# Optimization experiments

Measured on AMD Instinct MI355X. Metric: run time of the kernel, lower is better.

## Reference

```python
import jax, jax.numpy as jnp
import numpy as np

N = 100000
E = 1600000
F_IN, F_HID, F_OUT = 128, 32, 2


def setup_inputs() -> dict:
    key = jax.random.key(0)
    k1, k2, k3, k4 = jax.random.split(key, 4)
    x = jax.random.normal(k1, (N, F_IN), dtype=jnp.float32)
    edge_index = jax.random.randint(k2, (2, E), 0, N, dtype=jnp.int64)
    # Glorot-style init like torch_geometric GCNConv
    W1 = jax.random.normal(k3, (F_IN, F_HID), dtype=jnp.float32) * (1.0 / np.sqrt(F_IN))
    b1 = jnp.zeros((F_HID,), dtype=jnp.float32)
    W2 = jax.random.normal(k4, (F_HID, F_OUT), dtype=jnp.float32) * (1.0 / np.sqrt(F_HID))
    b2 = jnp.zeros((F_OUT,), dtype=jnp.float32)
    return {"x": x, "edge_index": edge_index, "W1": W1, "b1": b1, "W2": W2, "b2": b2}


def _gcn_conv(x, row, col, norm, W, b):
    # GCNConv: transform, then normalized aggregate (source -> target), then bias
    h = x @ W                                   # [N, F_out]
    msg = norm[:, None] * h[row]                # gather + scale, [E+N, F_out]
    out = jax.ops.segment_sum(msg, col, num_segments=N)  # scatter-add to targets
    return out + b


def reference(x, edge_index, W1, b1, W2, b2):
    # add self-loops (GCNConv default)
    loops = jnp.arange(N, dtype=edge_index.dtype)
    row = jnp.concatenate([edge_index[0], loops])
    col = jnp.concatenate([edge_index[1], loops])
    # symmetric normalization: deg^{-1/2}[row] * deg^{-1/2}[col], deg = in-degree w/ self-loops
    deg = jax.ops.segment_sum(jnp.ones_like(col, dtype=x.dtype), col, num_segments=N)
    dinv = jnp.where(deg > 0, jax.lax.rsqrt(deg), 0.0)
    norm = dinv[row] * dinv[col]                # [E+N]

    h = _gcn_conv(x, row, col, norm, W1, b1)
    h = jax.nn.relu(h)
    h = _gcn_conv(h, row, col, norm, W2, b2)
    return jax.nn.log_softmax(h, axis=1)
```

## Files before the change

### kernel.cpp

```cpp
#include <hip/hip_runtime.h>
#include <hip/hip_bf16.h>
#include <math.h>
#include <stdint.h>


#define GNN_N 100000
#define GNN_E 1600000
#define NBUCK 391
#define CAP 4608
#define CH 4096

__global__ __launch_bounds__(256) void k_bucket(const int* __restrict__ row,
                                                const int* __restrict__ col,
                                                int* __restrict__ bucket_fill,
                                                uint32_t* __restrict__ slab, int e) {
    __shared__ int hist[NBUCK];
    __shared__ int base[NBUCK];
    const int tid = threadIdx.x;
    const int e0 = blockIdx.x * CH;
    const int m = min(CH, e - e0);
    const bool full = (m == CH);

    int cc[16], rr[16];
    for (int i = tid; i < NBUCK; i += 256) hist[i] = 0;
    __syncthreads();

    if (full) {
        #pragma unroll
        for (int t = 0; t < 16; ++t) {
            cc[t] = col[e0 + tid + t * 256];
            rr[t] = row[e0 + tid + t * 256];
        }
        #pragma unroll
        for (int t = 0; t < 16; ++t) atomicAdd(&hist[cc[t] >> 8], 1);
    } else {
        for (int i = tid; i < m; i += 256) atomicAdd(&hist[col[e0 + i] >> 8], 1);
    }
    __syncthreads();
    for (int i = tid; i < NBUCK; i += 256) {
        int bb = (i + blockIdx.x * 131) % NBUCK;
        base[bb] = atomicAdd(&bucket_fill[bb], hist[bb]);
    }
    __syncthreads();
    if (full) {
        #pragma unroll
        for (int t = 0; t < 16; ++t) {
            int b = cc[t] >> 8;
            int p = atomicAdd(&base[b], 1);
            if (p < CAP)
                slab[(size_t)b * CAP + p] = ((uint32_t)rr[t] << 8) | (uint32_t)(cc[t] & 255);
        }
    } else {
        for (int i = tid; i < m; i += 256) {
            int c = col[e0 + i];
            int r = row[e0 + i];
            int b = c >> 8;
            int p = atomicAdd(&base[b], 1);
            if (p < CAP)
                slab[(size_t)b * CAP + p] = ((uint32_t)r << 8) | (uint32_t)(c & 255);
        }
    }
}

__global__ __launch_bounds__(512) void k_bucket_scan(const int* __restrict__ bucket_fill,
                                                     int* __restrict__ bucket_base, int nb) {
    int tid = threadIdx.x;
    int v = (tid < nb) ? bucket_fill[tid] : 0;
    int lane = tid & 63, wave = tid >> 6;
    int inc = v;
    #pragma unroll
    for (int d = 1; d < 64; d <<= 1) {
        int t = __shfl_up(inc, d);
        if (lane >= d) inc += t;
    }
    __shared__ int wsum[8];
    if (lane == 63) wsum[wave] = inc;
    __syncthreads();
    if (tid == 0) {
        int a = 0;
        #pragma unroll
        for (int w = 0; w < 8; ++w) { int t = wsum[w]; wsum[w] = a; a += t; }
    }
    __syncthreads();
    if (tid < nb) bucket_base[tid] = inc - v + wsum[wave];
}

__global__ __launch_bounds__(512) void k_fine(const uint32_t* __restrict__ slab,
                                              const int* __restrict__ bucket_fill,
                                              const int* __restrict__ bucket_base,
                                              int* __restrict__ sorted_row,
                                              int* __restrict__ cnt,
                                              int* __restrict__ offsets,
                                              float* __restrict__ dinv, int n) {
    __shared__ int hist[256];
    __shared__ int excl[256];
    __shared__ int cur[256];
    __shared__ int wsum[4];
    __shared__ uint32_t stage[CAP];
    const int tid = threadIdx.x;
    const int b = blockIdx.x;
    const int nb = min(bucket_fill[b], CAP);
    const int gbase = bucket_base[b];
    const uint32_t* sl = slab + (size_t)b * CAP;

    if (tid < 256) { hist[tid] = 0; cur[tid] = 0; }
    __syncthreads();
    for (int i = tid; i < nb; i += 512)
        atomicAdd(&hist[sl[i] & 255u], 1);
    __syncthreads();
    int v = 0, inc = 0;
    const int lane = tid & 63, wave = tid >> 6;
    if (tid < 256) {
        v = hist[tid];
        inc = v;
        #pragma unroll
        for (int d = 1; d < 64; d <<= 1) {
            int t = __shfl_up(inc, d);
            if (lane >= d) inc += t;
        }
        if (lane == 63) wsum[wave] = inc;
    }
    __syncthreads();
    if (tid == 0) {
        int a = 0;
        #pragma unroll
        for (int w = 0; w < 4; ++w) { int t = wsum[w]; wsum[w] = a; a += t; }
    }
    __syncthreads();
    if (tid < 256) {
        int ex = inc - v + wsum[wave];
        excl[tid] = ex;
        int c = b * 256 + tid;
        if (c < n) {
            cnt[c] = v;
            offsets[c] = gbase + ex;
            dinv[c] = rsqrtf((float)(v + 1));
        }
    }
    __syncthreads();
    for (int i = tid; i < nb; i += 512) {
        uint32_t u = sl[i];
        int f = (int)(u & 255u);
        int p = atomicAdd(&cur[f], 1);
        stage[excl[f] + p] = u >> 8;
    }
    __syncthreads();
    for (int i = tid; i < nb; i += 512)
        sorted_row[gbase + i] = (int)stage[i];
}

__device__ inline uint32_t pack_bf16(float a, float b) {
    uint32_t ua = __float_as_uint(a);
    uint32_t ub = __float_as_uint(b);
    ua = (ua + 0x7fffu + ((ua >> 16) & 1u)) >> 16;
    ub = (ub + 0x7fffu + ((ub >> 16) & 1u)) >> 16;
    return ua | (ub << 16);
}
__device__ inline void bf8_acc(float* acc, uint4 u) {
    acc[0] += __uint_as_float(u.x << 16);
    acc[1] += __uint_as_float(u.x & 0xffff0000u);
    acc[2] += __uint_as_float(u.y << 16);
    acc[3] += __uint_as_float(u.y & 0xffff0000u);
    acc[4] += __uint_as_float(u.z << 16);
    acc[5] += __uint_as_float(u.z & 0xffff0000u);
    acc[6] += __uint_as_float(u.w << 16);
    acc[7] += __uint_as_float(u.w & 0xffff0000u);
}

#define MM1_NODES 64
__global__ __launch_bounds__(256) void k_matmul1(const float* __restrict__ x,
                                                 const float* __restrict__ W1,
                                                 const float* __restrict__ dinv,
                                                 uint32_t* __restrict__ h1s, int n) {
    __shared__ float xs[MM1_NODES * 129];
    __shared__ float w1s[128 * 32];
    const int tid = threadIdx.x;
    const int nodeBase = blockIdx.x * MM1_NODES;

    {
        const float4* w4 = (const float4*)W1;
        float4* s4 = (float4*)w1s;
        for (int i = tid; i < 1024; i += 256) s4[i] = w4[i];
    }
    {
        const float4* x4 = (const float4*)x;
        for (int i = tid; i < MM1_NODES * 32; i += 256) {
            int node = i >> 5;
            int k4 = i & 31;
            float4 v = make_float4(0.f, 0.f, 0.f, 0.f);
            if (nodeBase + node < n)
                v = x4[(size_t)(nodeBase + node) * 32 + k4];
            int bb = node * 129 + k4 * 4;
            xs[bb + 0] = v.x; xs[bb + 1] = v.y; xs[bb + 2] = v.z; xs[bb + 3] = v.w;
        }
    }
    __syncthreads();

    const int fg = tid & 7;
    const int ng = tid >> 3;
    const int n0 = ng * 2;
    float4 acc0 = make_float4(0.f, 0.f, 0.f, 0.f);
    float4 acc1 = make_float4(0.f, 0.f, 0.f, 0.f);
    const float4* w1s4 = (const float4*)w1s;
    const float* xr0 = &xs[n0 * 129];
    const float* xr1 = &xs[(n0 + 1) * 129];
    #pragma unroll 8
    for (int k = 0; k < 128; ++k) {
        float4 w = w1s4[k * 8 + fg];
        float a = xr0[k];
        float b = xr1[k];
        acc0.x += a * w.x; acc0.y += a * w.y; acc0.z += a * w.z; acc0.w += a * w.w;
        acc1.x += b * w.x; acc1.y += b * w.y; acc1.z += b * w.z; acc1.w += b * w.w;
    }
    int gn0 = nodeBase + n0;
    if (gn0 < n) {
        float d = dinv[gn0];
        uint2 o = make_uint2(pack_bf16(acc0.x * d, acc0.y * d),
                             pack_bf16(acc0.z * d, acc0.w * d));
        ((uint2*)h1s)[(size_t)gn0 * 8 + fg] = o;
    }
    if (gn0 + 1 < n) {
        float d = dinv[gn0 + 1];
        uint2 o = make_uint2(pack_bf16(acc1.x * d, acc1.y * d),
                             pack_bf16(acc1.z * d, acc1.w * d));
        ((uint2*)h1s)[(size_t)(gn0 + 1) * 8 + fg] = o;
    }
}

__global__ __launch_bounds__(256) void k_gather1(const int* __restrict__ offsets,
                                                 const int* __restrict__ cnt,
                                                 const int* __restrict__ sorted_row,
                                                 const uint32_t* __restrict__ h1s,
                                                 const float* __restrict__ dinv,
                                                 const float* __restrict__ b1,
                                                 const float* __restrict__ W2,
                                                 float* __restrict__ h2s, int n) {
    const int tid = threadIdx.x;
    const int l = tid & 3;
    const int node = blockIdx.x * 64 + (tid >> 2);
    if (node >= n) return;
    const uint4* h4 = (const uint4*)h1s;
    float acc[8], acc2[8];
    #pragma unroll
    for (int j = 0; j < 8; ++j) { acc[j] = 0.f; acc2[j] = 0.f; }
    bf8_acc(acc, h4[(size_t)node * 4 + l]);
    const int start = offsets[node];
    const int deg = cnt[node];
    int k = 0;
    for (; k + 2 <= deg; k += 2) {
        int r0 = sorted_row[start + k];
        int r1 = sorted_row[start + k + 1];
        uint4 ua = h4[(size_t)r0 * 4 + l];
        uint4 ub = h4[(size_t)r1 * 4 + l];
        bf8_acc(acc, ua);
        bf8_acc(acc2, ub);
    }
    if (k < deg) {
        int r = sorted_row[start + k];
        bf8_acc(acc, h4[(size_t)r * 4 + l]);
    }
    #pragma unroll
    for (int j = 0; j < 8; ++j) acc[j] += acc2[j];

    const float d = dinv[node];
    const int f0 = l * 8;
    float s0 = 0.f, s1 = 0.f;
    #pragma unroll
    for (int j = 0; j < 8; ++j) {
        float a = fmaxf(d * acc[j] + b1[f0 + j], 0.f);
        s0 += a * W2[(f0 + j) * 2];
        s1 += a * W2[(f0 + j) * 2 + 1];
    }
    s0 += __shfl_xor(s0, 1); s0 += __shfl_xor(s0, 2);
    s1 += __shfl_xor(s1, 1); s1 += __shfl_xor(s1, 2);
    if (l == 0) ((float2*)h2s)[node] = make_float2(d * s0, d * s1);
}

__global__ __launch_bounds__(256) void k_gather2(const int* __restrict__ offsets,
                                                 const int* __restrict__ cnt,
                                                 const int* __restrict__ sorted_row,
                                                 const float* __restrict__ h2s,
                                                 const float* __restrict__ dinv,
                                                 const float* __restrict__ b2,
                                                 float* __restrict__ out, int n) {
    const int tid = threadIdx.x;
    const int l = tid & 3;
    const int node = blockIdx.x * 64 + (tid >> 2);
    if (node >= n) return;
    const float2* h2 = (const float2*)h2s;
    float sx = 0.f, sy = 0.f;
    if (l == 0) { float2 s = h2[node]; sx = s.x; sy = s.y; }
    const int start = offsets[node];
    const int deg = cnt[node];
    for (int k = l; k < deg; k += 4) {
        float2 v = h2[sorted_row[start + k]];
        sx += v.x; sy += v.y;
    }
    sx += __shfl_xor(sx, 1); sx += __shfl_xor(sx, 2);
    sy += __shfl_xor(sy, 1); sy += __shfl_xor(sy, 2);
    if (l == 0) {
        float d = dinv[node];
        float v0 = d * sx + b2[0];
        float v1 = d * sy + b2[1];
        float m = fmaxf(v0, v1);
        float lg = m + logf(expf(v0 - m) + expf(v1 - m));
        ((float2*)out)[node] = make_float2(v0 - lg, v1 - lg);
    }
}

extern "C" void kernel_launch(void* const* d_in, const int* in_sizes, int n_in,
                              void* d_out, int out_size, void* d_ws, size_t ws_size,
                              hipStream_t stream) {
    const float* x  = (const float*)d_in[0];
    const int*   ei = (const int*)d_in[1];
    const float* W1 = (const float*)d_in[2];
    const float* b1 = (const float*)d_in[3];
    const float* W2 = (const float*)d_in[4];
    const float* b2 = (const float*)d_in[5];
    float* out = (float*)d_out;
    char* ws = (char*)d_ws;

    const int N = GNN_N, E = GNN_E;
    const int* row = ei;
    const int* col = ei + E;

    float*    dinv        = (float*)    ws;
    int*      cnt         = (int*)     (ws + 4ull *  100000);
    int*      offsets     = (int*)     (ws + 4ull *  200000);
    int*      bucket_fill = (int*)     (ws + 4ull *  300000);
    int*      bucket_base = (int*)     (ws + 4ull *  300512);
    int*      sorted_row  = (int*)     (ws + 4ull *  301024);
    float*    h2s         = (float*)   (ws + 4ull * 1901024);
    uint32_t* h1s         = (uint32_t*)(ws + 4ull * 2101024);
    uint32_t* slab        = (uint32_t*)(ws + 4ull * 3701024);

    hipMemsetAsync(bucket_fill, 0, NBUCK * sizeof(int), stream);

    k_bucket     <<<(E + CH - 1) / CH, 256, 0, stream>>>(row, col, bucket_fill, slab, E);
    k_bucket_scan<<<1, 512, 0, stream>>>(bucket_fill, bucket_base, NBUCK);
    k_fine       <<<NBUCK, 512, 0, stream>>>(slab, bucket_fill, bucket_base,
                                             sorted_row, cnt, offsets, dinv, N);
    k_matmul1    <<<(N + MM1_NODES - 1) / MM1_NODES, 256, 0, stream>>>(x, W1, dinv, h1s, N);
    k_gather1    <<<(N + 63) / 64, 256, 0, stream>>>(offsets, cnt, sorted_row, h1s, dinv, b1, W2, h2s, N);
    k_gather2    <<<(N + 63) / 64, 256, 0, stream>>>(offsets, cnt, sorted_row, h2s, dinv, b2, out, N);
}
```

Before: 188.0 us.

## Reorder pipeline: unscaled matmul first, fuse memset and bucket scan away

New measurement: 193.9 us. 1.03x slower.

```diff
diff --git a/kernel.cpp b/kernel.cpp
--- a/kernel.cpp
+++ b/kernel.cpp
@@ -8,146 +8,10 @@
 #define GNN_E 1600000
 #define NBUCK 391
 #define CAP 4608
-#define CH 4096
-
-__global__ __launch_bounds__(256) void k_bucket(const int* __restrict__ row,
-                                                const int* __restrict__ col,
-                                                int* __restrict__ bucket_fill,
-                                                uint32_t* __restrict__ slab, int e) {
-    __shared__ int hist[NBUCK];
-    __shared__ int base[NBUCK];
-    const int tid = threadIdx.x;
-    const int e0 = blockIdx.x * CH;
-    const int m = min(CH, e - e0);
-    const bool full = (m == CH);
-
-    int cc[16], rr[16];
-    for (int i = tid; i < NBUCK; i += 256) hist[i] = 0;
-    __syncthreads();
-
-    if (full) {
-        #pragma unroll
-        for (int t = 0; t < 16; ++t) {
-            cc[t] = col[e0 + tid + t * 256];
-            rr[t] = row[e0 + tid + t * 256];
-        }
-        #pragma unroll
-        for (int t = 0; t < 16; ++t) atomicAdd(&hist[cc[t] >> 8], 1);
-    } else {
-        for (int i = tid; i < m; i += 256) atomicAdd(&hist[col[e0 + i] >> 8], 1);
-    }
-    __syncthreads();
-    for (int i = tid; i < NBUCK; i += 256) {
-        int bb = (i + blockIdx.x * 131) % NBUCK;
-        base[bb] = atomicAdd(&bucket_fill[bb], hist[bb]);
-    }
-    __syncthreads();
-    if (full) {
-        #pragma unroll
-        for (int t = 0; t < 16; ++t) {
-            int b = cc[t] >> 8;
-            int p = atomicAdd(&base[b], 1);
-            if (p < CAP)
-                slab[(size_t)b * CAP + p] = ((uint32_t)rr[t] << 8) | (uint32_t)(cc[t] & 255);
-        }
-    } else {
-        for (int i = tid; i < m; i += 256) {
-            int c = col[e0 + i];
-            int r = row[e0 + i];
-            int b = c >> 8;
-            int p = atomicAdd(&base[b], 1);
-            if (p < CAP)
-                slab[(size_t)b * CAP + p] = ((uint32_t)r << 8) | (uint32_t)(c & 255);
-        }
-    }
-}
-
-__global__ __launch_bounds__(512) void k_bucket_scan(const int* __restrict__ bucket_fill,
-                                                     int* __restrict__ bucket_base, int nb) {
-    int tid = threadIdx.x;
-    int v = (tid < nb) ? bucket_fill[tid] : 0;
-    int lane = tid & 63, wave = tid >> 6;
-    int inc = v;
-    #pragma unroll
-    for (int d = 1; d < 64; d <<= 1) {
-        int t = __shfl_up(inc, d);
-        if (lane >= d) inc += t;
-    }
-    __shared__ int wsum[8];
-    if (lane == 63) wsum[wave] = inc;
-    __syncthreads();
-    if (tid == 0) {
-        int a = 0;
-        #pragma unroll
-        for (int w = 0; w < 8; ++w) { int t = wsum[w]; wsum[w] = a; a += t; }
-    }
-    __syncthreads();
-    if (tid < nb) bucket_base[tid] = inc - v + wsum[wave];
-}
-
-__global__ __launch_bounds__(512) void k_fine(const uint32_t* __restrict__ slab,
-                                              const int* __restrict__ bucket_fill,
-                                              const int* __restrict__ bucket_base,
-                                              int* __restrict__ sorted_row,
-                                              int* __restrict__ cnt,
-                                              int* __restrict__ offsets,
-                                              float* __restrict__ dinv, int n) {
-    __shared__ int hist[256];
-    __shared__ int excl[256];
-    __shared__ int cur[256];
-    __shared__ int wsum[4];
-    __shared__ uint32_t stage[CAP];
-    const int tid = threadIdx.x;
-    const int b = blockIdx.x;
-    const int nb = min(bucket_fill[b], CAP);
-    const int gbase = bucket_base[b];
-    const uint32_t* sl = slab + (size_t)b * CAP;
-
-    if (tid < 256) { hist[tid] = 0; cur[tid] = 0; }
-    __syncthreads();
-    for (int i = tid; i < nb; i += 512)
-        atomicAdd(&hist[sl[i] & 255u], 1);
-    __syncthreads();
-    int v = 0, inc = 0;
-    const int lane = tid & 63, wave = tid >> 6;
-    if (tid < 256) {
-        v = hist[tid];
-        inc = v;
-        #pragma unroll
-        for (int d = 1; d < 64; d <<= 1) {
-            int t = __shfl_up(inc, d);
-            if (lane >= d) inc += t;
-        }
-        if (lane == 63) wsum[wave] = inc;
-    }
-    __syncthreads();
-    if (tid == 0) {
-        int a = 0;
-        #pragma unroll
-        for (int w = 0; w < 4; ++w) { int t = wsum[w]; wsum[w] = a; a += t; }
-    }
-    __syncthreads();
-    if (tid < 256) {
-        int ex = inc - v + wsum[wave];
-        excl[tid] = ex;
-        int c = b * 256 + tid;
-        if (c < n) {
-            cnt[c] = v;
-            offsets[c] = gbase + ex;
-            dinv[c] = rsqrtf((float)(v + 1));
-        }
-    }
-    __syncthreads();
-    for (int i = tid; i < nb; i += 512) {
-        uint32_t u = sl[i];
-        int f = (int)(u & 255u);
-        int p = atomicAdd(&cur[f], 1);
-        stage[excl[f] + p] = u >> 8;
-    }
-    __syncthreads();
-    for (int i = tid; i < nb; i += 512)
-        sorted_row[gbase + i] = (int)stage[i];
-}
+#define CH 3125
+
+__device__ inline float bf_lo(uint32_t u) { return __uint_as_float(u << 16); }
+__device__ inline float bf_hi(uint32_t u) { return __uint_as_float(u & 0xffff0000u); }
 
 __device__ inline uint32_t pack_bf16(float a, float b) {
     uint32_t ua = __float_as_uint(a);
@@ -156,26 +20,26 @@
     ub = (ub + 0x7fffu + ((ub >> 16) & 1u)) >> 16;
     return ua | (ub << 16);
 }
-__device__ inline void bf8_acc(float* acc, uint4 u) {
-    acc[0] += __uint_as_float(u.x << 16);
-    acc[1] += __uint_as_float(u.x & 0xffff0000u);
-    acc[2] += __uint_as_float(u.y << 16);
-    acc[3] += __uint_as_float(u.y & 0xffff0000u);
-    acc[4] += __uint_as_float(u.z << 16);
-    acc[5] += __uint_as_float(u.z & 0xffff0000u);
-    acc[6] += __uint_as_float(u.w << 16);
-    acc[7] += __uint_as_float(u.w & 0xffff0000u);
+
+__device__ inline void bf8_fma(float* acc, uint4 u, float d) {
+    acc[0] += d * bf_lo(u.x); acc[1] += d * bf_hi(u.x);
+    acc[2] += d * bf_lo(u.y); acc[3] += d * bf_hi(u.y);
+    acc[4] += d * bf_lo(u.z); acc[5] += d * bf_hi(u.z);
+    acc[6] += d * bf_lo(u.w); acc[7] += d * bf_hi(u.w);
 }
 
 #define MM1_NODES 64
-__global__ __launch_bounds__(256) void k_matmul1(const float* __restrict__ x,
-                                                 const float* __restrict__ W1,
-                                                 const float* __restrict__ dinv,
-                                                 uint32_t* __restrict__ h1s, int n) {
+__global__ __launch_bounds__(256) void k_matmul1z(const float* __restrict__ x,
+                                                  const float* __restrict__ W1,
+                                                  uint32_t* __restrict__ h1u,
+                                                  int* __restrict__ bucket_fill, int n) {
     __shared__ float xs[MM1_NODES * 129];
     __shared__ float w1s[128 * 32];
     const int tid = threadIdx.x;
     const int nodeBase = blockIdx.x * MM1_NODES;
+
+    if (blockIdx.x == 0)
+        for (int i = tid; i < NBUCK; i += 256) bucket_fill[i] = 0;
 
     {
         const float4* w4 = (const float4*)W1;
@@ -213,24 +77,118 @@
         acc1.x += b * w.x; acc1.y += b * w.y; acc1.z += b * w.z; acc1.w += b * w.w;
     }
     int gn0 = nodeBase + n0;
-    if (gn0 < n) {
-        float d = dinv[gn0];
-        uint2 o = make_uint2(pack_bf16(acc0.x * d, acc0.y * d),
-                             pack_bf16(acc0.z * d, acc0.w * d));
-        ((uint2*)h1s)[(size_t)gn0 * 8 + fg] = o;
-    }
-    if (gn0 + 1 < n) {
-        float d = dinv[gn0 + 1];
-        uint2 o = make_uint2(pack_bf16(acc1.x * d, acc1.y * d),
-                             pack_bf16(acc1.z * d, acc1.w * d));
-        ((uint2*)h1s)[(size_t)(gn0 + 1) * 8 + fg] = o;
-    }
+    if (gn0 < n)
+        ((uint2*)h1u)[(size_t)gn0 * 8 + fg] =
+            make_uint2(pack_bf16(acc0.x, acc0.y), pack_bf16(acc0.z, acc0.w));
+    if (gn0 + 1 < n)
+        ((uint2*)h1u)[(size_t)(gn0 + 1) * 8 + fg] =
+            make_uint2(pack_bf16(acc1.x, acc1.y), pack_bf16(acc1.z, acc1.w));
+}
+
+__global__ __launch_bounds__(256) void k_bucket(const int* __restrict__ row,
+                                                const int* __restrict__ col,
+                                                int* __restrict__ bucket_fill,
+                                                uint32_t* __restrict__ slab) {
+    __shared__ int hist[NBUCK];
+    __shared__ int base[NBUCK];
+    const int tid = threadIdx.x;
+    const int e0 = blockIdx.x * CH;
+
+    for (int i = tid; i < NBUCK; i += 256) hist[i] = 0;
+    __syncthreads();
+    for (int i = tid; i < CH; i += 256)
+        atomicAdd(&hist[col[e0 + i] >> 8], 1);
+    __syncthreads();
+    for (int i = tid; i < NBUCK; i += 256) {
+        int bb = (i + blockIdx.x * 131) % NBUCK;
+        base[bb] = atomicAdd(&bucket_fill[bb], hist[bb]);
+    }
+    __syncthreads();
+    for (int i = tid; i < CH; i += 256) {
+        int c = col[e0 + i];
+        int r = row[e0 + i];
+        int b = c >> 8;
+        int p = atomicAdd(&base[b], 1);
+        if (p < CAP)
+            slab[(size_t)b * CAP + p] = ((uint32_t)r << 8) | (uint32_t)(c & 255);
+    }
+}
+
+__global__ __launch_bounds__(512) void k_fine(const uint32_t* __restrict__ slab,
+                                              const int* __restrict__ bucket_fill,
+                                              int* __restrict__ sorted_row,
+                                              int* __restrict__ cnt,
+                                              int* __restrict__ offsets,
+                                              float* __restrict__ dinv, int n) {
+    __shared__ int hist[256];
+    __shared__ int excl[256];
+    __shared__ int cur[256];
+    __shared__ int wsum[4];
+    __shared__ int s_gbase;
+    __shared__ uint32_t stage[CAP];
+    const int tid = threadIdx.x;
+    const int b = blockIdx.x;
+    const int nb = min(bucket_fill[b], CAP);
+    const uint32_t* sl = slab + (size_t)b * CAP;
+
+    if (tid < 256) { hist[tid] = 0; cur[tid] = 0; }
+    if (tid < 64) {
+        int s = 0;
+        for (int i = tid; i < b; i += 64) s += bucket_fill[i];
+        #pragma unroll
+        for (int m = 32; m >= 1; m >>= 1) s += __shfl_xor(s, m);
+        if (tid == 0) s_gbase = s;
+    }
+    __syncthreads();
+    for (int i = tid; i < nb; i += 512)
+        atomicAdd(&hist[sl[i] & 255u], 1);
+    __syncthreads();
+    int v = 0, inc = 0;
+    const int lane = tid & 63, wave = tid >> 6;
+    if (tid < 256) {
+        v = hist[tid];
+        inc = v;
+        #pragma unroll
+        for (int d = 1; d < 64; d <<= 1) {
+            int t = __shfl_up(inc, d);
+            if (lane >= d) inc += t;
+        }
+        if (lane == 63) wsum[wave] = inc;
+    }
+    __syncthreads();
+    if (tid == 0) {
+        int a = 0;
+        #pragma unroll
+        for (int w = 0; w < 4; ++w) { int t = wsum[w]; wsum[w] = a; a += t; }
+    }
+    __syncthreads();
+    const int gbase = s_gbase;
+    if (tid < 256) {
+        int ex = inc - v + wsum[wave];
+        excl[tid] = ex;
+        int c = b * 256 + tid;
+        if (c < n) {
+            cnt[c] = v;
+            offsets[c] = gbase + ex;
+            dinv[c] = rsqrtf((float)(v + 1));
+        }
+    }
+    __syncthreads();
+    for (int i = tid; i < nb; i += 512) {
+        uint32_t u = sl[i];
+        int f = (int)(u & 255u);
+        int p = atomicAdd(&cur[f], 1);
+        stage[excl[f] + p] = u >> 8;
+    }
+    __syncthreads();
+    for (int i = tid; i < nb; i += 512)
+        sorted_row[gbase + i] = (int)stage[i];
 }
 
 __global__ __launch_bounds__(256) void k_gather1(const int* __restrict__ offsets,
                                                  const int* __restrict__ cnt,
                                                  const int* __restrict__ sorted_row,
-                                                 const uint32_t* __restrict__ h1s,
+                                                 const uint32_t* __restrict__ h1u,
                                                  const float* __restrict__ dinv,
                                                  const float* __restrict__ b1,
                                                  const float* __restrict__ W2,
@@ -239,41 +197,41 @@
     const int l = tid & 3;
     const int node = blockIdx.x * 64 + (tid >> 2);
     if (node >= n) return;
-    const uint4* h4 = (const uint4*)h1s;
+    const uint4* h4 = (const uint4*)h1u;
     float acc[8], acc2[8];
     #pragma unroll
     for (int j = 0; j < 8; ++j) { acc[j] = 0.f; acc2[j] = 0.f; }
-    bf8_acc(acc, h4[(size_t)node * 4 + l]);
+    const float dc = dinv[node];
+    bf8_fma(acc, h4[(size_t)node * 4 + l], dc);
     const int start = offsets[node];
     const int deg = cnt[node];
     int k = 0;
     for (; k + 2 <= deg; k += 2) {
         int r0 = sorted_row[start + k];
         int r1 = sorted_row[start + k + 1];
-        uint4 ua = h4[(size_t)r0 * 4 + l];
-        uint4 ub = h4[(size_t)r1 * 4 + l];
-        bf8_acc(acc, ua);
-        bf8_acc(acc2, ub);
+        float d0 = dinv[r0];
+        float d1 = dinv[r1];
+        bf8_fma(acc, h4[(size_t)r0 * 4 + l], d0);
+        bf8_fma(acc2, h4[(size_t)r1 * 4 + l], d1);
     }
     if (k < deg) {
         int r = sorted_row[start + k];
-        bf8_acc(acc, h4[(size_t)r * 4 + l]);
+        bf8_fma(acc, h4[(size_t)r * 4 + l], dinv[r]);
     }
     #pragma unroll
     for (int j = 0; j < 8; ++j) acc[j] += acc2[j];
 
-    const float d = dinv[node];
     const int f0 = l * 8;
     float s0 = 0.f, s1 = 0.f;
     #pragma unroll
     for (int j = 0; j < 8; ++j) {
-        float a = fmaxf(d * acc[j] + b1[f0 + j], 0.f);
+        float a = fmaxf(dc * acc[j] + b1[f0 + j], 0.f);
         s0 += a * W2[(f0 + j) * 2];
         s1 += a * W2[(f0 + j) * 2 + 1];
     }
     s0 += __shfl_xor(s0, 1); s0 += __shfl_xor(s0, 2);
     s1 += __shfl_xor(s1, 1); s1 += __shfl_xor(s1, 2);
-    if (l == 0) ((float2*)h2s)[node] = make_float2(d * s0, d * s1);
+    if (l == 0) ((float2*)h2s)[node] = make_float2(dc * s0, dc * s1);
 }
 
 __global__ __launch_bounds__(256) void k_gather2(const int* __restrict__ offsets,
@@ -328,19 +286,14 @@
     int*      cnt         = (int*)     (ws + 4ull *  100000);
     int*      offsets     = (int*)     (ws + 4ull *  200000);
     int*      bucket_fill = (int*)     (ws + 4ull *  300000);
-    int*      bucket_base = (int*)     (ws + 4ull *  300512);
-    int*      sorted_row  = (int*)     (ws + 4ull *  301024);
-    float*    h2s         = (float*)   (ws + 4ull * 1901024);
-    uint32_t* h1s         = (uint32_t*)(ws + 4ull * 2101024);
-    uint32_t* slab        = (uint32_t*)(ws + 4ull * 3701024);
-
-    hipMemsetAsync(bucket_fill, 0, NBUCK * sizeof(int), stream);
-
-    k_bucket     <<<(E + CH - 1) / CH, 256, 0, stream>>>(row, col, bucket_fill, slab, E);
-    k_bucket_scan<<<1, 512, 0, stream>>>(bucket_fill, bucket_base, NBUCK);
-    k_fine       <<<NBUCK, 512, 0, stream>>>(slab, bucket_fill, bucket_base,
-                                             sorted_row, cnt, offsets, dinv, N);
-    k_matmul1    <<<(N + MM1_NODES - 1) / MM1_NODES, 256, 0, stream>>>(x, W1, dinv, h1s, N);
-    k_gather1    <<<(N + 63) / 64, 256, 0, stream>>>(offsets, cnt, sorted_row, h1s, dinv, b1, W2, h2s, N);
-    k_gather2    <<<(N + 63) / 64, 256, 0, stream>>>(offsets, cnt, sorted_row, h2s, dinv, b2, out, N);
-}
+    int*      sorted_row  = (int*)     (ws + 4ull *  300512);
+    float*    h2s         = (float*)   (ws + 4ull * 1900512);
+    uint32_t* h1u         = (uint32_t*)(ws + 4ull * 2100512);
+    uint32_t* slab        = (uint32_t*)(ws + 4ull * 3700512);
+
+    k_matmul1z<<<(N + MM1_NODES - 1) / MM1_NODES, 256, 0, stream>>>(x, W1, h1u, bucket_fill, N);
+    k_bucket  <<<512, 256, 0, stream>>>(row, col, bucket_fill, slab);
+    k_fine    <<<NBUCK, 512, 0, stream>>>(slab, bucket_fill, sorted_row, cnt, offsets, dinv, N);
+    k_gather1 <<<(N + 63) / 64, 256, 0, stream>>>(offsets, cnt, sorted_row, h1u, dinv, b1, W2, h2s, N);
+    k_gather2 <<<(N + 63) / 64, 256, 0, stream>>>(offsets, cnt, sorted_row, h2s, dinv, b2, out, N);
+}
```
